# Kernel optimization log

Hardware: AMD Instinct MI355X
Metric: run time of the kernel (lower is better)

## Reference

```python
import jax, jax.numpy as jnp
import numpy as np

NUM_HEADS = 16
KEY_SIZE = 64
VALUE_SIZE = 64
D_MODEL = 1024
B, S = 2, 2048

def setup_inputs() -> dict:
    key = jax.random.key(0)
    k1, k2 = jax.random.split(key)
    inputs = jax.random.normal(k1, (B, S, D_MODEL), dtype=jnp.float32)
    qkv_width = NUM_HEADS * (KEY_SIZE + KEY_SIZE + VALUE_SIZE)  # 3072
    W = jax.random.normal(k2, (D_MODEL, qkv_width), dtype=jnp.float32) / np.sqrt(D_MODEL)
    b = jnp.zeros((qkv_width,), dtype=jnp.float32)
    return {"inputs": inputs, "W": W, "b": b}

def reference(inputs, W, b):
    # Fused QKV projection: [B, S, H*(2k+v)]
    qkv = jnp.einsum("bsd,de->bse", inputs, W) + b
    Bsz, S_ = inputs.shape[0], inputs.shape[1]
    qkv = qkv.reshape(Bsz, S_, NUM_HEADS, 2 * KEY_SIZE + VALUE_SIZE)
    qkv = jnp.transpose(qkv, (0, 2, 1, 3))  # [B, H, S, 2k+v]
    q = qkv[..., :KEY_SIZE]
    k = qkv[..., KEY_SIZE:2 * KEY_SIZE]
    v = qkv[..., 2 * KEY_SIZE:]
    # NOTE: original multiplies by sqrt(key_size) (not divide) -- faithful.
    scores = jnp.einsum("bhqd,bhkd->bhqk", q, k) * jnp.sqrt(jnp.float32(KEY_SIZE))
    weights = jax.nn.softmax(scores, axis=-1)
    out = jnp.einsum("bhqk,bhkv->bhqv", weights, v)  # [B, H, S, v]
    out = jnp.transpose(out, (0, 2, 1, 3)).reshape(Bsz, S_, NUM_HEADS * VALUE_SIZE)
    return out
```

## Files before the change

kernel.cpp:

```cpp
#include <hip/hip_runtime.h>


#define S_LEN 2048
#define NH    16
#define DH    64
#define DM    1024
#define EW    3072
#define NROWS 4096
#define NT    32

#define QSCALE 11.5415603f

using f32x4 = __attribute__((ext_vector_type(4))) float;
using bf8   = __attribute__((ext_vector_type(8))) short;
using s4v   = __attribute__((ext_vector_type(4))) short;

static __device__ __forceinline__ short f2bf(float f) {
  union { float f; unsigned u; } a; a.f = f;
  unsigned r = a.u + 0x7fffu + ((a.u >> 16) & 1u);
  return (short)(r >> 16);
}
static __device__ __forceinline__ float bf2f(short h) {
  union { float f; unsigned u; } a;
  a.u = ((unsigned)(unsigned short)h) << 16;
  return a.f;
}
static __device__ __forceinline__ unsigned fbits(float f) {
  union { float f; unsigned u; } a; a.f = f; return a.u;
}
static __device__ __forceinline__ void gl16(const void* g, void* l) {
  __builtin_amdgcn_global_load_lds(
      (const __attribute__((address_space(1))) void*)g,
      (__attribute__((address_space(3))) void*)l, 16, 0, 0);
}

__global__ __launch_bounds__(256) void prep_x(const float* __restrict__ X,
                                              short* __restrict__ Xh,
                                              short* __restrict__ Xl) {
  int i = blockIdx.x * 256 + threadIdx.x;
  float4 v = ((const float4*)X)[i];
  s4v h, l;
  h.x = f2bf(v.x); l.x = f2bf(v.x - bf2f(h.x));
  h.y = f2bf(v.y); l.y = f2bf(v.y - bf2f(h.y));
  h.z = f2bf(v.z); l.z = f2bf(v.z - bf2f(h.z));
  h.w = f2bf(v.w); l.w = f2bf(v.w - bf2f(h.w));
  ((s4v*)Xh)[i] = h;
  ((s4v*)Xl)[i] = l;
}

__global__ __launch_bounds__(256) void prep_w(const float* __restrict__ W,
                                              short* __restrict__ Wth,
                                              short* __restrict__ Wtl) {
  __shared__ float t[32][33];
  int n0 = blockIdx.x * 32;
  int k0 = blockIdx.y * 32;
  int tx = threadIdx.x & 31;
  int ty = threadIdx.x >> 5;
#pragma unroll
  for (int i = 0; i < 32; i += 8)
    t[ty + i][tx] = W[(size_t)(k0 + ty + i) * EW + n0 + tx];
  __syncthreads();
#pragma unroll
  for (int i = 0; i < 32; i += 8) {
    float v = t[tx][ty + i];
    short hi = f2bf(v);
    short lo = f2bf(v - bf2f(hi));
    size_t o = (size_t)(n0 + ty + i) * DM + k0 + tx;
    Wth[o] = hi; Wtl[o] = lo;
  }
}

__global__ __launch_bounds__(256, 2) void proj(
    const short* __restrict__ Xh, const short* __restrict__ Xl,
    const short* __restrict__ Wth, const short* __restrict__ Wtl,
    const float* __restrict__ bias,
    short* __restrict__ Qh, short* __restrict__ Ql,
    short* __restrict__ Kh, short* __restrict__ Kl,
    short* __restrict__ Vt) {
  __shared__ short Ah[2][4096], Al[2][4096], Bh[2][4096], Bl[2][4096];
  const int tid = threadIdx.x;
  const int lane = tid & 63, w = tid >> 6;
  const int wr = w >> 1, wc = w & 1;
  const int c = lane & 15, g = lane >> 4;

  const int id = blockIdx.x;
  const int rowBase = (((id & 7) << 2) + ((id >> 3) & 3)) * 128;
  const int colBase = (id >> 5) * 128;

  f32x4 acc[4][4] = {};

  const int sr  = 32 * w + (lane >> 2);
  const int csw = ((lane & 3) ^ ((lane >> 3) & 3)) * 8;
  const int ldsw = w * 1024;
  const size_t aBase = (size_t)(rowBase + sr) * DM + csw;
  const size_t bBase = (size_t)(colBase + sr) * DM + csw;

  const int rsw = (g ^ ((c >> 1) & 3)) * 8;

#define PSTAGE(B, kt) do {                                    \
    gl16(&Xh[aBase + (kt)],            &Ah[B][ldsw]);         \
    gl16(&Xh[aBase + (kt) + 16 * DM],  &Ah[B][ldsw + 512]);   \
    gl16(&Xl[aBase + (kt)],            &Al[B][ldsw]);         \
    gl16(&Xl[aBase + (kt) + 16 * DM],  &Al[B][ldsw + 512]);   \
    gl16(&Wth[bBase + (kt)],           &Bh[B][ldsw]);         \
    gl16(&Wth[bBase + (kt) + 16 * DM], &Bh[B][ldsw + 512]);   \
    gl16(&Wtl[bBase + (kt)],           &Bl[B][ldsw]);         \
    gl16(&Wtl[bBase + (kt) + 16 * DM], &Bl[B][ldsw + 512]);   \
  } while (0)

  PSTAGE(0, 0);
  __syncthreads();

  for (int it = 0; it < 32; ++it) {
    const int cur = it & 1;
    if (it + 1 < 32) PSTAGE(cur ^ 1, (it + 1) * 32);

    bf8 ah[4], al4[4], bh[4], bl[4];
#pragma unroll
    for (int m = 0; m < 4; ++m) {
      int ro = (wr * 64 + m * 16 + c) * 32 + rsw;
      ah[m]  = *(const bf8*)&Ah[cur][ro];
      al4[m] = *(const bf8*)&Al[cur][ro];
    }
#pragma unroll
    for (int n = 0; n < 4; ++n) {
      int ro = (wc * 64 + n * 16 + c) * 32 + rsw;
      bh[n] = *(const bf8*)&Bh[cur][ro];
      bl[n] = *(const bf8*)&Bl[cur][ro];
    }
    __builtin_amdgcn_s_setprio(1);
#pragma unroll
    for (int m = 0; m < 4; ++m)
#pragma unroll
      for (int n = 0; n < 4; ++n) {
        acc[m][n] = __builtin_amdgcn_mfma_f32_16x16x32_bf16(al4[m], bh[n], acc[m][n], 0, 0, 0);
        acc[m][n] = __builtin_amdgcn_mfma_f32_16x16x32_bf16(ah[m], bl[n], acc[m][n], 0, 0, 0);
        acc[m][n] = __builtin_amdgcn_mfma_f32_16x16x32_bf16(ah[m], bh[n], acc[m][n], 0, 0, 0);
      }
    __builtin_amdgcn_s_setprio(0);
    __syncthreads();
  }
#undef PSTAGE

#pragma unroll
  for (int m = 0; m < 4; ++m)
#pragma unroll
    for (int n = 0; n < 4; ++n)
#pragma unroll
      for (int j = 0; j < 4; ++j) {
        int grow = rowBase + wr * 64 + m * 16 + g * 4 + j;
        int gcol = colBase + wc * 64 + n * 16 + c;
        float v = acc[m][n][j] + bias[gcol];
        int bb = grow >> 11, s = grow & 2047;
        int h = gcol / 192, e = gcol - h * 192;
        size_t hb = (size_t)(bb * NH + h);
        if (e < DH) {
          float q8 = v * QSCALE;
          short hi = f2bf(q8);
          short lo = f2bf(q8 - bf2f(hi));
          size_t idx = (hb * S_LEN + s) * DH + e;
          Qh[idx] = hi; Ql[idx] = lo;
        } else if (e < 2 * DH) {
          short hi = f2bf(v);
          short lo = f2bf(v - bf2f(hi));
          int tile = s >> 6, r = s & 63, d = e - DH;
          size_t idx = ((hb * NT + tile) * (size_t)4096) + r * 64 +
                       ((((d >> 3) ^ (r & 7)) << 3) | (d & 7));
          Kh[idx] = hi; Kl[idx] = lo;
        } else {
          int tile = s >> 6, key = s & 63, d = e - 2 * DH;
          int kc = key >> 5, g4 = (key >> 2) & 3;
          int ii = (((key >> 4) & 1) << 2) | (key & 3);
          size_t idx = ((hb * NT + tile) * (size_t)4096) + d * 64 +
                       (((((kc << 2) | g4) ^ (d & 7)) << 3) | ii);
          Vt[idx] = f2bf(v);
        }
      }
}

__global__ __launch_bounds__(512, 4) void attn(
    const short* __restrict__ Qh, const short* __restrict__ Ql,
    const short* __restrict__ KhG, const short* __restrict__ KlG,
    const short* __restrict__ VtG, float* __restrict__ out) {
  __shared__ short KHs[2][4096];
  __shared__ short KLs[2][4096];
  __shared__ short Vs[2][4096];

  const int tid = threadIdx.x;
  const int lane = tid & 63, w = tid >> 6;
  const int c = lane & 15, g = lane >> 4;
  const int id = blockIdx.x;
  const int lid = (id & 7) * 64 + (id >> 3);
  const int bh = lid >> 4;
  const int q0 = (lid & 15) * 128 + w * 16;
  const size_t qBase  = (size_t)bh * S_LEN * DH;
  const size_t kvBase = (size_t)bh * NT * 4096;

  const int seg = tid * 8;

  bf8 qh[2], ql[2];
#pragma unroll
  for (int kc = 0; kc < 2; ++kc) {
    size_t idx = qBase + (size_t)(q0 + c) * DH + kc * 32 + g * 8;
    qh[kc] = *(const bf8*)&Qh[idx];
    ql[kc] = *(const bf8*)&Ql[idx];
  }

  int koff[2][4];
#pragma unroll
  for (int kc = 0; kc < 2; ++kc)
#pragma unroll
    for (int i = 0; i < 4; ++i)
      koff[kc][i] = (i * 16 + c) * 64 + (((kc * 4 + g) ^ (c & 7)) << 3);

  float mrun = -INFINITY, lpart = 0.f;
  f32x4 o[4] = {};

  gl16(&KhG[kvBase + seg], &KHs[0][seg]);
  gl16(&KlG[kvBase + seg], &KLs[0][seg]);
  gl16(&VtG[kvBase + seg], &Vs[0][seg]);
  __syncthreads();

  for (int t = 0; t < NT; ++t) {
    const int cur = t & 1, nxt = cur ^ 1;
    if (t + 1 < NT) {
      size_t tb = kvBase + (size_t)(t + 1) * 4096 + seg;
      gl16(&KhG[tb], &KHs[nxt][seg]);
      gl16(&KlG[tb], &KLs[nxt][seg]);
      gl16(&VtG[tb], &Vs[nxt][seg]);
    }
    const short* KH = &KHs[cur][0];
    const short* KL = &KLs[cur][0];
    const short* VV = &Vs[cur][0];

    f32x4 sc[4];
    __builtin_amdgcn_s_setprio(1);
#pragma unroll
    for (int nb = 0; nb < 4; ++nb) {
      f32x4 s = {};
#pragma unroll
      for (int kc = 0; kc < 2; ++kc) {
        bf8 kh = *(const bf8*)&KH[koff[kc][nb]];
        bf8 kl = *(const bf8*)&KL[koff[kc][nb]];
        s = __builtin_amdgcn_mfma_f32_16x16x32_bf16(kh, ql[kc], s, 0, 0, 0);
        s = __builtin_amdgcn_mfma_f32_16x16x32_bf16(kl, qh[kc], s, 0, 0, 0);
        s = __builtin_amdgcn_mfma_f32_16x16x32_bf16(kh, qh[kc], s, 0, 0, 0);
      }
      sc[nb] = s;
    }
    __builtin_amdgcn_s_setprio(0);

    float m0 = fmaxf(fmaxf(sc[0][0], sc[0][1]), fmaxf(sc[0][2], sc[0][3]));
#pragma unroll
    for (int nb = 1; nb < 4; ++nb)
      m0 = fmaxf(m0, fmaxf(fmaxf(sc[nb][0], sc[nb][1]),
                           fmaxf(sc[nb][2], sc[nb][3])));
    m0 = fmaxf(m0, __shfl_xor(m0, 16));
    m0 = fmaxf(m0, __shfl_xor(m0, 32));

    if (__any(m0 > mrun + 8.0f)) {
      float mnew = fmaxf(mrun, m0);
      float scale = exp2f(mrun - mnew);
      mrun = mnew;
      lpart *= scale;
      int sb = (g << 4) | (g << 2);
      float s0 = __shfl(scale, sb);
      float s1 = __shfl(scale, sb + 1);
      float s2 = __shfl(scale, sb + 2);
      float s3 = __shfl(scale, sb + 3);
#pragma unroll
      for (int db = 0; db < 4; ++db) {
        o[db][0] *= s0; o[db][1] *= s1; o[db][2] *= s2; o[db][3] *= s3;
      }
    }

#pragma unroll
    for (int nb = 0; nb < 4; ++nb)
#pragma unroll
      for (int j = 0; j < 4; ++j)
        sc[nb][j] = exp2f(sc[nb][j] - mrun);
#pragma unroll
    for (int nb = 0; nb < 4; ++nb)
      lpart += (sc[nb][0] + sc[nb][1]) + (sc[nb][2] + sc[nb][3]);

    union { bf8 v; unsigned u[4]; } pa[2];
#pragma unroll
    for (int kc = 0; kc < 2; ++kc) {
      pa[kc].u[0] = (fbits(sc[2*kc][0]) >> 16)   | (fbits(sc[2*kc][1])   & 0xffff0000u);
      pa[kc].u[1] = (fbits(sc[2*kc][2]) >> 16)   | (fbits(sc[2*kc][3])   & 0xffff0000u);
      pa[kc].u[2] = (fbits(sc[2*kc+1][0]) >> 16) | (fbits(sc[2*kc+1][1]) & 0xffff0000u);
      pa[kc].u[3] = (fbits(sc[2*kc+1][2]) >> 16) | (fbits(sc[2*kc+1][3]) & 0xffff0000u);
    }

    __builtin_amdgcn_s_setprio(1);
#pragma unroll
    for (int kc = 0; kc < 2; ++kc)
#pragma unroll
      for (int db = 0; db < 4; ++db) {
        bf8 vb = *(const bf8*)&VV[koff[kc][db]];
        o[db] = __builtin_amdgcn_mfma_f32_16x16x32_bf16(pa[kc].v, vb, o[db], 0, 0, 0);
      }
    __builtin_amdgcn_s_setprio(0);

    __syncthreads();
  }

  lpart += __shfl_xor(lpart, 16);
  lpart += __shfl_xor(lpart, 32);
  int sb = (g << 4) | (g << 2);
  float r0 = 1.f / __shfl(lpart, sb);
  float r1 = 1.f / __shfl(lpart, sb + 1);
  float r2 = 1.f / __shfl(lpart, sb + 2);
  float r3 = 1.f / __shfl(lpart, sb + 3);

  const int b = bh >> 4, h = bh & 15;
#pragma unroll
  for (int db = 0; db < 4; ++db) {
    int col = h * DH + db * 16 + c;
    out[((size_t)b * S_LEN + q0 + g * 4 + 0) * DM + col] = o[db][0] * r0;
    out[((size_t)b * S_LEN + q0 + g * 4 + 1) * DM + col] = o[db][1] * r1;
    out[((size_t)b * S_LEN + q0 + g * 4 + 2) * DM + col] = o[db][2] * r2;
    out[((size_t)b * S_LEN + q0 + g * 4 + 3) * DM + col] = o[db][3] * r3;
  }
}

extern "C" void kernel_launch(void* const* d_in, const int* in_sizes, int n_in,
                              void* d_out, int out_size, void* d_ws, size_t ws_size,
                              hipStream_t stream) {
  const float* X    = (const float*)d_in[0];
  const float* W    = (const float*)d_in[1];
  const float* bias = (const float*)d_in[2];
  float* out = (float*)d_out;

  char* ws = (char*)d_ws;
  size_t off = 0;
  auto take = [&](size_t bytes) {
    void* p = ws + off;
    off += (bytes + 255) & ~(size_t)255;
    return p;
  };
  short* Xh  = (short*)take((size_t)NROWS * DM * 2);
  short* Xl  = (short*)take((size_t)NROWS * DM * 2);
  short* Wth = (short*)take((size_t)EW * DM * 2);
  short* Wtl = (short*)take((size_t)EW * DM * 2);
  short* Qh  = (short*)take((size_t)2 * NH * S_LEN * DH * 2);
  short* Ql  = (short*)take((size_t)2 * NH * S_LEN * DH * 2);
  short* Kh  = (short*)take((size_t)2 * NH * NT * 4096 * 2);
  short* Kl  = (short*)take((size_t)2 * NH * NT * 4096 * 2);
  short* Vt  = (short*)take((size_t)2 * NH * NT * 4096 * 2);

  prep_x<<<dim3(4096), dim3(256), 0, stream>>>(X, Xh, Xl);
  prep_w<<<dim3(EW / 32, DM / 32), dim3(256), 0, stream>>>(W, Wth, Wtl);
  proj<<<dim3(768), dim3(256), 0, stream>>>(
      Xh, Xl, Wth, Wtl, bias, Qh, Ql, Kh, Kl, Vt);
  attn<<<dim3(512), dim3(512), 0, stream>>>(
      Qh, Ql, Kh, Kl, Vt, out);
}
```

Measured before the change: 195.3 us.

## Split projection into QK split-bf16 GEMM and single-bf16 V GEMM

Permutes the transposed weight columns so Q, K and V occupy contiguous column ranges. The projection is split into two kernels: a Q/K kernel that keeps the 3-MFMA hi/lo split-bf16 emulation, and a V kernel that uses only hi parts, with one MFMA and half the loads. The target is the wasted precision work on V, which the attention kernel stores as plain bf16 anyway. The next-stage prefetch is also moved after the LDS fragment reads, and there is now one extra kernel launch. V loses the low-order product terms before rounding.

```diff
diff --git a/kernel.cpp b/kernel.cpp
--- a/kernel.cpp
+++ b/kernel.cpp
@@ -63,20 +63,24 @@
 #pragma unroll
   for (int i = 0; i < 32; i += 8) {
     float v = t[tx][ty + i];
+    int n = n0 + ty + i;
+    int h = n / 192, e = n - h * 192;
+    int np = (e < 64) ? (h * 64 + e)
+           : (e < 128) ? (1024 + h * 64 + (e - 64))
+                       : (2048 + h * 64 + (e - 128));
     short hi = f2bf(v);
     short lo = f2bf(v - bf2f(hi));
-    size_t o = (size_t)(n0 + ty + i) * DM + k0 + tx;
+    size_t o = (size_t)np * DM + k0 + tx;
     Wth[o] = hi; Wtl[o] = lo;
   }
 }
 
-__global__ __launch_bounds__(256, 2) void proj(
+__global__ __launch_bounds__(256, 2) void proj_qk(
     const short* __restrict__ Xh, const short* __restrict__ Xl,
     const short* __restrict__ Wth, const short* __restrict__ Wtl,
     const float* __restrict__ bias,
     short* __restrict__ Qh, short* __restrict__ Ql,
-    short* __restrict__ Kh, short* __restrict__ Kl,
-    short* __restrict__ Vt) {
+    short* __restrict__ Kh, short* __restrict__ Kl) {
   __shared__ short Ah[2][4096], Al[2][4096], Bh[2][4096], Bl[2][4096];
   const int tid = threadIdx.x;
   const int lane = tid & 63, w = tid >> 6;
@@ -84,8 +88,9 @@
   const int c = lane & 15, g = lane >> 4;
 
   const int id = blockIdx.x;
-  const int rowBase = (((id & 7) << 2) + ((id >> 3) & 3)) * 128;
-  const int colBase = (id >> 5) * 128;
+  const int t = id >> 3;
+  const int rowBase = (((id & 7) << 2) + (t & 3)) * 128;
+  const int colBase = (t >> 2) * 128;
 
   f32x4 acc[4][4] = {};
 
@@ -113,7 +118,6 @@
 
   for (int it = 0; it < 32; ++it) {
     const int cur = it & 1;
-    if (it + 1 < 32) PSTAGE(cur ^ 1, (it + 1) * 32);
 
     bf8 ah[4], al4[4], bh[4], bl[4];
 #pragma unroll
@@ -128,6 +132,8 @@
       bh[n] = *(const bf8*)&Bh[cur][ro];
       bl[n] = *(const bf8*)&Bl[cur][ro];
     }
+    if (it + 1 < 32) PSTAGE(cur ^ 1, (it + 1) * 32);
+
     __builtin_amdgcn_s_setprio(1);
 #pragma unroll
     for (int m = 0; m < 4; ++m)
@@ -150,31 +156,100 @@
       for (int j = 0; j < 4; ++j) {
         int grow = rowBase + wr * 64 + m * 16 + g * 4 + j;
         int gcol = colBase + wc * 64 + n * 16 + c;
-        float v = acc[m][n][j] + bias[gcol];
+        int h = (gcol >> 6) & 15, e = gcol & 63;
         int bb = grow >> 11, s = grow & 2047;
-        int h = gcol / 192, e = gcol - h * 192;
         size_t hb = (size_t)(bb * NH + h);
-        if (e < DH) {
-          float q8 = v * QSCALE;
+        if (gcol < 1024) {
+          float q8 = (acc[m][n][j] + bias[h * 192 + e]) * QSCALE;
           short hi = f2bf(q8);
           short lo = f2bf(q8 - bf2f(hi));
           size_t idx = (hb * S_LEN + s) * DH + e;
           Qh[idx] = hi; Ql[idx] = lo;
-        } else if (e < 2 * DH) {
+        } else {
+          float v = acc[m][n][j] + bias[h * 192 + 64 + e];
           short hi = f2bf(v);
           short lo = f2bf(v - bf2f(hi));
-          int tile = s >> 6, r = s & 63, d = e - DH;
+          int tile = s >> 6, r = s & 63;
           size_t idx = ((hb * NT + tile) * (size_t)4096) + r * 64 +
-                       ((((d >> 3) ^ (r & 7)) << 3) | (d & 7));
+                       ((((e >> 3) ^ (r & 7)) << 3) | (e & 7));
           Kh[idx] = hi; Kl[idx] = lo;
-        } else {
-          int tile = s >> 6, key = s & 63, d = e - 2 * DH;
-          int kc = key >> 5, g4 = (key >> 2) & 3;
-          int ii = (((key >> 4) & 1) << 2) | (key & 3);
-          size_t idx = ((hb * NT + tile) * (size_t)4096) + d * 64 +
-                       (((((kc << 2) | g4) ^ (d & 7)) << 3) | ii);
-          Vt[idx] = f2bf(v);
         }
+      }
+}
+
+__global__ __launch_bounds__(256, 2) void proj_v(
+    const short* __restrict__ Xh, const short* __restrict__ Wth,
+    const float* __restrict__ bias, short* __restrict__ Vt) {
+  __shared__ short Ah[2][4096], Bh[2][4096];
+  const int tid = threadIdx.x;
+  const int lane = tid & 63, w = tid >> 6;
+  const int wr = w >> 1, wc = w & 1;
+  const int c = lane & 15, g = lane >> 4;
+
+  const int id = blockIdx.x;
+  const int t = id >> 3;
+  const int rowBase = (((id & 7) << 2) + (t & 3)) * 128;
+  const int colBase = 2048 + (t >> 2) * 128;
+
+  f32x4 acc[4][4] = {};
+
+  const int sr  = 32 * w + (lane >> 2);
+  const int csw = ((lane & 3) ^ ((lane >> 3) & 3)) * 8;
+  const int ldsw = w * 1024;
+  const size_t aBase = (size_t)(rowBase + sr) * DM + csw;
+  const size_t bBase = (size_t)(colBase + sr) * DM + csw;
+  const int rsw = (g ^ ((c >> 1) & 3)) * 8;
+
+#define VSTAGE(B, kt) do {                                    \
+    gl16(&Xh[aBase + (kt)],            &Ah[B][ldsw]);         \
+    gl16(&Xh[aBase + (kt) + 16 * DM],  &Ah[B][ldsw + 512]);   \
+    gl16(&Wth[bBase + (kt)],           &Bh[B][ldsw]);         \
+    gl16(&Wth[bBase + (kt) + 16 * DM], &Bh[B][ldsw + 512]);   \
+  } while (0)
+
+  VSTAGE(0, 0);
+  __syncthreads();
+
+  for (int it = 0; it < 32; ++it) {
+    const int cur = it & 1;
+    bf8 ah[4], bh[4];
+#pragma unroll
+    for (int m = 0; m < 4; ++m)
+      ah[m] = *(const bf8*)&Ah[cur][(wr * 64 + m * 16 + c) * 32 + rsw];
+#pragma unroll
+    for (int n = 0; n < 4; ++n)
+      bh[n] = *(const bf8*)&Bh[cur][(wc * 64 + n * 16 + c) * 32 + rsw];
+    if (it + 1 < 32) VSTAGE(cur ^ 1, (it + 1) * 32);
+
+    __builtin_amdgcn_s_setprio(1);
+#pragma unroll
+    for (int m = 0; m < 4; ++m)
+#pragma unroll
+      for (int n = 0; n < 4; ++n)
+        acc[m][n] = __builtin_amdgcn_mfma_f32_16x16x32_bf16(ah[m], bh[n], acc[m][n], 0, 0, 0);
+    __builtin_amdgcn_s_setprio(0);
+    __syncthreads();
+  }
+#undef VSTAGE
+
+#pragma unroll
+  for (int m = 0; m < 4; ++m)
+#pragma unroll
+    for (int n = 0; n < 4; ++n)
+#pragma unroll
+      for (int j = 0; j < 4; ++j) {
+        int grow = rowBase + wr * 64 + m * 16 + g * 4 + j;
+        int gcol = colBase + wc * 64 + n * 16 + c;
+        int h = (gcol >> 6) & 15, d = gcol & 63;
+        int bb = grow >> 11, s = grow & 2047;
+        size_t hb = (size_t)(bb * NH + h);
+        float v = acc[m][n][j] + bias[h * 192 + 128 + d];
+        int tile = s >> 6, key = s & 63;
+        int kc = key >> 5, g4 = (key >> 2) & 3;
+        int ii = (((key >> 4) & 1) << 2) | (key & 3);
+        size_t idx = ((hb * NT + tile) * (size_t)4096) + d * 64 +
+                     (((((kc << 2) | g4) ^ (d & 7)) << 3) | ii);
+        Vt[idx] = f2bf(v);
       }
 }
 
@@ -351,8 +426,9 @@
 
   prep_x<<<dim3(4096), dim3(256), 0, stream>>>(X, Xh, Xl);
   prep_w<<<dim3(EW / 32, DM / 32), dim3(256), 0, stream>>>(W, Wth, Wtl);
-  proj<<<dim3(768), dim3(256), 0, stream>>>(
-      Xh, Xl, Wth, Wtl, bias, Qh, Ql, Kh, Kl, Vt);
+  proj_qk<<<dim3(512), dim3(256), 0, stream>>>(
+      Xh, Xl, Wth, Wtl, bias, Qh, Ql, Kh, Kl);
+  proj_v<<<dim3(256), dim3(256), 0, stream>>>(Xh, Wth, bias, Vt);
   attn<<<dim3(512), dim3(512), 0, stream>>>(
       Qh, Ql, Kh, Kl, Vt, out);
 }
```

Result: faster. 174.5 us (-10.6%).
